# Kernel tuning notes

Hardware: AMD Instinct MI355X
Metric: run time of the kernel (lower is better)

## Reference

```python
import jax, jax.numpy as jnp
import numpy as np

N_NODES = 100000
N_EDGES = 3200000
D_IN = 256
D_HID = 97


def setup_inputs() -> dict:
    key = jax.random.key(0)
    k1, k2, k3, k4, k5, k6 = jax.random.split(key, 6)
    x = jax.random.normal(k1, (N_NODES, D_IN), dtype=jnp.float32)
    edge_index = jax.random.randint(k2, (2, N_EDGES), 0, N_NODES, dtype=jnp.int64)
    # GCNConv weights (stored as [in, out]) and biases
    W1 = jax.random.normal(k3, (D_IN, D_HID), dtype=jnp.float32) / np.sqrt(D_IN)
    b1 = jnp.zeros((D_HID,), dtype=jnp.float32)
    W2 = jax.random.normal(k4, (D_HID, D_HID), dtype=jnp.float32) / np.sqrt(D_HID)
    b2 = jnp.zeros((D_HID,), dtype=jnp.float32)
    return {"x": x, "edge_index": edge_index, "W1": W1, "b1": b1, "W2": W2, "b2": b2}


def reference(x, edge_index, W1, b1, W2, b2):
    # PyG GCNConv: add self-loops, symmetric degree normalization,
    # out[i] = sum_j norm_ij * (x[j] @ W) + b
    N = x.shape[0]
    self_idx = jnp.arange(N, dtype=edge_index.dtype)
    src = jnp.concatenate([edge_index[0], self_idx])  # source j
    dst = jnp.concatenate([edge_index[1], self_idx])  # target i
    deg = jax.ops.segment_sum(jnp.ones_like(dst, dtype=x.dtype), dst, num_segments=N)
    dinv = jnp.where(deg > 0, 1.0 / jnp.sqrt(deg), 0.0)
    norm = dinv[src] * dinv[dst]  # [E+N]

    def gcn(h, W, b):
        h = h @ W  # dense linear transform first (out_dim small)
        msg = h[src] * norm[:, None]  # gather + scale
        agg = jax.ops.segment_sum(msg, dst, num_segments=N)  # scatter-add
        return agg + b

    h = jax.nn.relu(gcn(x, W1, b1))
    out = gcn(h, W2, b2)
    return out
```

## Files before the change

### kernel.cpp

```cpp
#include <hip/hip_runtime.h>
#include <hip/hip_fp16.h>
#include <stdint.h>

#define D_IN 256
#define D_H  97
#define RST  96
#define NPB  512
#define NBMAX 256
#define CHUNK 4096
#define KP1  264
#define KP2  136

typedef _Float16 f16;
typedef f16   f16x8 __attribute__((ext_vector_type(8)));
typedef float f32x4 __attribute__((ext_vector_type(4)));

__device__ __forceinline__ int load_idx(const void* p, int is64, long long pos) {
  if (is64) return (int)(((const long long*)p)[pos]);
  return ((const int*)p)[pos];
}

__global__ void detect_kernel(const void* ei, long long E, int* flag) {
  const int* p32 = (const int*)ei;
  long long stride = E / 1024; if (stride < 1) stride = 1;
  int tid = threadIdx.x;
  int bad = 0;
  for (int s = 0; s < 4; ++s) {
    long long k = ((long long)tid * 4 + s) * stride;
    if (k < E) {
      if (p32[2 * k + 1] != 0) bad = 1;
    }
  }
  __shared__ int sh_bad;
  if (tid == 0) sh_bad = 0;
  __syncthreads();
  if (bad) atomicOr(&sh_bad, 1);
  __syncthreads();
  if (tid == 0) *flag = sh_bad ? 0 : 1;
}

__global__ __launch_bounds__(256) void bucket_scatter_direct(
    const void* ei, const int* __restrict__ flag, int* __restrict__ bcur,
    unsigned int* __restrict__ bsd, long long E, int nbuck, int cap) {
  __shared__ unsigned int packs[CHUNK];
  __shared__ unsigned char bkts[CHUNK];
  __shared__ int hist[NBMAX];
  __shared__ int gpos[NBMAX];
  __shared__ int cur[NBMAX];
  int tid = threadIdx.x;
  if (tid < NBMAX) { hist[tid] = 0; cur[tid] = 0; }
  __syncthreads();
  int f = *flag;
  long long base = (long long)blockIdx.x * CHUNK;
  int cnt = (int)((E - base < CHUNK) ? (E - base) : CHUNK);
  #pragma unroll 4
  for (int i = tid; i < cnt; i += 256) {
    long long e = base + i;
    int s = load_idx(ei, f, e);
    int d = load_idx(ei, f, E + e);
    int b = d >> 9;
    packs[i] = ((unsigned int)(d & (NPB - 1)) << 17) | (unsigned int)s;
    bkts[i] = (unsigned char)b;
    atomicAdd(&hist[b], 1);
  }
  __syncthreads();
  if (tid < nbuck) { int h = hist[tid]; if (h) gpos[tid] = atomicAdd(&bcur[tid], h); }
  __syncthreads();
  #pragma unroll 4
  for (int i = tid; i < cnt; i += 256) {
    int b = bkts[i];
    int r = atomicAdd(&cur[b], 1);
    int idx = gpos[b] + r;
    if (idx < cap) bsd[(size_t)b * cap + idx] = packs[i];
  }
}

__global__ void bucket_scan2(const int* __restrict__ bcur, int* __restrict__ bstart,
                             int* __restrict__ row_start, int N, int nbuck, int cap) {
  __shared__ int sh[256];
  int tid = threadIdx.x;
  int v = (tid < nbuck) ? min(bcur[tid], cap) : 0;
  sh[tid] = v;
  __syncthreads();
  for (int off = 1; off < 256; off <<= 1) {
    int a = (tid >= off) ? sh[tid - off] : 0;
    __syncthreads();
    sh[tid] += a;
    __syncthreads();
  }
  if (tid < nbuck) bstart[tid] = sh[tid] - v;
  if (tid == 255) { bstart[nbuck] = sh[255]; row_start[N] = sh[255]; }
}

__global__ __launch_bounds__(256) void bucket_finalize(
    const unsigned int* __restrict__ bsd, const int* __restrict__ bcur,
    const int* __restrict__ bstart,
    int* __restrict__ row_start, float* __restrict__ dinv,
    int* __restrict__ csr_src, int N, int cap) {
  __shared__ int h[NPB];
  __shared__ int rs[NPB];
  __shared__ int cur[NPB];
  __shared__ int wsum[4];
  int b = blockIdx.x, tid = threadIdx.x;
  int lane = tid & 63, wid = tid >> 6;
  h[2 * tid] = 0; h[2 * tid + 1] = 0;
  cur[2 * tid] = 0; cur[2 * tid + 1] = 0;
  __syncthreads();
  int d0 = b * cap;
  int cnt = min(bcur[b], cap);
  for (int i = tid; i < cnt; i += 256) atomicAdd(&h[bsd[d0 + i] >> 17], 1);
  __syncthreads();
  int a0 = h[2 * tid], a1 = h[2 * tid + 1];
  int tsum = a0 + a1;
  int incl = tsum;
  #pragma unroll
  for (int off = 1; off < 64; off <<= 1) {
    int n = __shfl_up(incl, off, 64);
    if (lane >= off) incl += n;
  }
  if (lane == 63) wsum[wid] = incl;
  __syncthreads();
  int woff = 0;
  for (int k = 0; k < wid; ++k) woff += wsum[k];
  int excl = woff + incl - tsum + bstart[b];
  rs[2 * tid] = excl;
  rs[2 * tid + 1] = excl + a0;
  int node0 = b * NPB;
  int n0 = node0 + 2 * tid, n1 = node0 + 2 * tid + 1;
  if (n0 < N) { row_start[n0] = excl;      dinv[n0] = rsqrtf((float)(a0 + 1)); }
  if (n1 < N) { row_start[n1] = excl + a0; dinv[n1] = rsqrtf((float)(a1 + 1)); }
  __syncthreads();
  for (int i = tid; i < cnt; i += 256) {
    unsigned int p = bsd[d0 + i];
    int r = p >> 17;
    int s = (int)(p & 0x1FFFFu);
    int rel = atomicAdd(&cur[r], 1);
    csr_src[rs[r] + rel] = s;
  }
}

__global__ void prep_kernel(const float* __restrict__ W1, const float* __restrict__ b1,
                            const float* __restrict__ W2, const float* __restrict__ b2,
                            f16* __restrict__ W1t, f16* __restrict__ W2t,
                            float* __restrict__ b1p, float* __restrict__ b2p) {
  int idx = blockIdx.x * blockDim.x + threadIdx.x;
  const int n1 = 112 * KP1, n2 = 112 * KP2;
  if (idx < n1) {
    int c = idx / KP1, k = idx % KP1;
    W1t[idx] = (f16)((c < D_H && k < 256) ? W1[k * D_H + c] : 0.f);
  } else if (idx < n1 + n2) {
    int j = idx - n1; int c = j / KP2, k = j % KP2;
    W2t[j] = (f16)((c < D_H && k < D_H) ? W2[k * D_H + c] : 0.f);
  } else if (idx < n1 + n2 + 128) {
    int c = idx - (n1 + n2);
    b1p[c] = (c < D_H) ? b1[c] : 0.0f;
  } else if (idx < n1 + n2 + 256) {
    int c = idx - (n1 + n2 + 128);
    b2p[c] = (c < D_H) ? b2[c] : 0.0f;
  }
}

template<int KI, int KP, bool IN_HALF>
__global__ __launch_bounds__(256) void mfma_gemm(
    const void* __restrict__ Av, const __half2* __restrict__ sideA,
    const f16* __restrict__ Wt, const float* __restrict__ dinv,
    __half* __restrict__ C, __half2* __restrict__ sideC, int N) {
  __shared__ f16 Bs[112 * KP];
  __shared__ f16 As[128 * 40];
  int tid = threadIdx.x;
  int wave = tid >> 6, lane = tid & 63;
  int row0 = blockIdx.x * 128;

  for (int i = tid * 8; i < 112 * KP; i += 2048)
    *(f16x8*)&Bs[i] = *(const f16x8*)&Wt[i];

  f32x4 acc[2][7];
  #pragma unroll
  for (int mg = 0; mg < 2; ++mg)
    #pragma unroll
    for (int cg = 0; cg < 7; ++cg)
      #pragma unroll
      for (int j = 0; j < 4; ++j) acc[mg][cg][j] = 0.f;

  for (int kb = 0; kb < KI; ++kb) {
    if (kb) __syncthreads();
    int k0 = kb * 32;
    if constexpr (!IN_HALF) {
      #pragma unroll
      for (int ii = 0; ii < 4; ++ii) {
        int i = tid + ii * 256;
        int row = i >> 3, col = (i & 7) * 4;
        int gr = row0 + row;
        float4 v = make_float4(0.f, 0.f, 0.f, 0.f);
        if (gr < N) v = *(const float4*)&((const float*)Av)[(size_t)gr * 256 + k0 + col];
        __half2* dst = (__half2*)&As[row * 40 + col];
        dst[0] = __floats2half2_rn(v.x, v.y);
        dst[1] = __floats2half2_rn(v.z, v.w);
      }
    } else {
      if (kb < KI - 1) {
        #pragma unroll
        for (int ii = 0; ii < 2; ++ii) {
          int i = tid + ii * 256;
          int row = i >> 2, col = (i & 3) * 8;
          int gr = row0 + row;
          f16x8 v;
          #pragma unroll
          for (int q = 0; q < 8; ++q) v[q] = (f16)0.f;
          if (gr < N) v = *(const f16x8*)&((const f16*)Av)[(size_t)gr * RST + k0 + col];
          *(f16x8*)&As[row * 40 + col] = v;
        }
      } else {
        if (tid < 128) {
          int gr = row0 + tid;
          f16 sv = (f16)0.f;
          if (gr < N) sv = ((const f16*)sideA)[2 * gr];
          f16* dst = &As[tid * 40];
          #pragma unroll
          for (int q = 0; q < 32; ++q) dst[q] = (f16)0.f;
          dst[0] = sv;
        }
      }
    }
    __syncthreads();
    int rbase = wave * 32 + (lane & 15);
    int kf = (lane >> 4) * 8;
    f16x8 a0 = *(const f16x8*)&As[rbase * 40 + kf];
    f16x8 a1 = *(const f16x8*)&As[(rbase + 16) * 40 + kf];
    #pragma unroll
    for (int cg = 0; cg < 7; ++cg) {
      f16x8 b = *(const f16x8*)&Bs[(cg * 16 + (lane & 15)) * KP + k0 + kf];
      acc[0][cg] = __builtin_amdgcn_mfma_f32_16x16x32_f16(a0, b, acc[0][cg], 0, 0, 0);
      acc[1][cg] = __builtin_amdgcn_mfma_f32_16x16x32_f16(a1, b, acc[1][cg], 0, 0, 0);
    }
  }
  int colb = lane & 15, rq = (lane >> 4) * 4;
  #pragma unroll
  for (int mg = 0; mg < 2; ++mg) {
    #pragma unroll
    for (int j = 0; j < 4; ++j) {
      int r = row0 + wave * 32 + mg * 16 + rq + j;
      if (r >= N) continue;
      float dv = dinv[r];
      #pragma unroll
      for (int cg = 0; cg < 7; ++cg) {
        int c = cg * 16 + colb;
        float val = acc[mg][cg][j] * dv;
        if (c < 96)       C[(size_t)r * RST + c] = __float2half(val);
        else if (c == 96) sideC[r] = __floats2half2_rn(val, 0.f);
      }
    }
  }
}

template<bool OUT_HALF, bool DO_RELU>
__global__ __launch_bounds__(256) void agg_kernel(
    const __half* __restrict__ t, const __half2* __restrict__ side,
    const int* __restrict__ csr_src, const int* __restrict__ row_start,
    const float* __restrict__ dinv, const float* __restrict__ bias,
    void* __restrict__ outp, __half2* __restrict__ side_out, int N) {
  int lane = threadIdx.x & 63;
  int node = blockIdx.x * (blockDim.x >> 6) + (threadIdx.x >> 6);
  if (node >= N || lane >= 49) return;
  const char* gbase = (lane < 48) ? (const char*)t + lane * 4 : (const char*)side;
  unsigned gscale = (lane < 48) ? (unsigned)(RST * 2) : 4u;
  auto GATHER = [&](int j) -> float2 {
    return __half22float2(*(const __half2*)(gbase + (size_t)((unsigned)j * gscale)));
  };
  int s = row_start[node], epd = row_start[node + 1];
  float di = dinv[node];
  float2 v = GATHER(node);
  float ax = v.x, ay = v.y;
  int e = s;
  while ((e & 3) && e < epd) {
    float2 u = GATHER(csr_src[e]);
    ax += u.x; ay += u.y; ++e;
  }
  for (; e + 8 <= epd; e += 8) {
    int4 q0 = *(const int4*)(csr_src + e);
    int4 q1 = *(const int4*)(csr_src + e + 4);
    float2 u0 = GATHER(q0.x), u1 = GATHER(q0.y), u2 = GATHER(q0.z), u3 = GATHER(q0.w);
    float2 u4 = GATHER(q1.x), u5 = GATHER(q1.y), u6 = GATHER(q1.z), u7 = GATHER(q1.w);
    ax += ((u0.x + u1.x) + (u2.x + u3.x)) + ((u4.x + u5.x) + (u6.x + u7.x));
    ay += ((u0.y + u1.y) + (u2.y + u3.y)) + ((u4.y + u5.y) + (u6.y + u7.y));
  }
  if (e + 4 <= epd) {
    int4 q0 = *(const int4*)(csr_src + e);
    float2 u0 = GATHER(q0.x), u1 = GATHER(q0.y), u2 = GATHER(q0.z), u3 = GATHER(q0.w);
    ax += (u0.x + u1.x) + (u2.x + u3.x);
    ay += (u0.y + u1.y) + (u2.y + u3.y);
    e += 4;
  }
  for (; e < epd; ++e) {
    float2 u = GATHER(csr_src[e]);
    ax += u.x; ay += u.y;
  }
  int c0 = 2 * lane;
  ax = ax * di + bias[c0];
  ay = ay * di + bias[c0 + 1];
  if (DO_RELU) { ax = fmaxf(ax, 0.f); ay = fmaxf(ay, 0.f); }
  if (OUT_HALF) {
    if (lane < 48) ((__half2*)((__half*)outp + (size_t)node * RST))[lane] = __floats2half2_rn(ax, ay);
    else           side_out[node] = __floats2half2_rn(ax, 0.f);
  } else {
    float* o = (float*)outp + (size_t)node * D_H;
    if (lane < 48) { o[c0] = ax; o[c0 + 1] = ay; }
    else           o[96] = ax;
  }
}

extern "C" void kernel_launch(void* const* d_in, const int* in_sizes, int n_in,
                              void* d_out, int out_size, void* d_ws, size_t ws_size,
                              hipStream_t stream) {
  const float* x  = (const float*)d_in[0];
  const void*  ei = d_in[1];
  const float* W1 = (const float*)d_in[2];
  const float* b1 = (const float*)d_in[3];
  const float* W2 = (const float*)d_in[4];
  const float* b2 = (const float*)d_in[5];
  int N = in_sizes[0] / D_IN;
  long long E = (long long)in_sizes[1] / 2;
  int nbuck = (N + NPB - 1) / NPB;
  int cap = (int)(E / nbuck) + 8192;

  char* base = (char*)d_ws;
  size_t off = 0;
  auto alloc = [&](size_t bytes) -> void* {
    void* p = base + off;
    off = (off + bytes + 255) & ~(size_t)255;
    return p;
  };
  int*    flag      = (int*)alloc(4);
  float*  dinv      = (float*)alloc((size_t)N * 4);
  int*    row_start = (int*)alloc((size_t)(N + 1) * 4);
  int*    bcur      = (int*)alloc((size_t)(nbuck + 1) * 4);
  int*    bstart    = (int*)alloc((size_t)(nbuck + 1) * 4);
  int*    csr_src   = (int*)alloc((size_t)E * 4);
  unsigned int* bsd = (unsigned int*)alloc((size_t)nbuck * cap * 4);
  f16*    W1t       = (f16*)alloc((size_t)112 * KP1 * 2);
  f16*    W2t       = (f16*)alloc((size_t)112 * KP2 * 2);
  float*  b1p       = (float*)alloc(128 * 4);
  float*  b2p       = (float*)alloc(128 * 4);
  __half* t1        = (__half*)alloc((size_t)N * RST * 2 + 256);
  __half2* sideT    = (__half2*)alloc((size_t)N * 4 + 256);
  __half* h1        = (__half*)alloc((size_t)N * RST * 2 + 256);
  __half2* sideH    = (__half2*)alloc((size_t)N * 4 + 256);

  hipMemsetAsync(bcur, 0, (size_t)(nbuck + 1) * 4, stream);
  detect_kernel<<<1, 256, 0, stream>>>(ei, E, flag);
  bucket_scatter_direct<<<(int)((E + CHUNK - 1) / CHUNK), 256, 0, stream>>>(
      ei, flag, bcur, bsd, E, nbuck, cap);
  bucket_scan2<<<1, 256, 0, stream>>>(bcur, bstart, row_start, N, nbuck, cap);
  bucket_finalize<<<nbuck, 256, 0, stream>>>(bsd, bcur, bstart, row_start, dinv, csr_src, N, cap);
  prep_kernel<<<(112 * KP1 + 112 * KP2 + 256 + 255) / 256, 256, 0, stream>>>(
      W1, b1, W2, b2, W1t, W2t, b1p, b2p);
  mfma_gemm<8, KP1, false><<<(N + 127) / 128, 256, 0, stream>>>(
      x, nullptr, W1t, dinv, t1, sideT, N);
  agg_kernel<true, true><<<(N + 3) / 4, 256, 0, stream>>>(t1, sideT, csr_src, row_start,
                                                          dinv, b1p, h1, sideH, N);
  mfma_gemm<4, KP2, true><<<(N + 127) / 128, 256, 0, stream>>>(
      h1, sideH, W2t, dinv, t1, sideT, N);
  agg_kernel<false, false><<<(N + 3) / 4, 256, 0, stream>>>(t1, sideT, csr_src, row_start,
                                                            dinv, b2p, d_out, nullptr, N);
}
```

Baseline: 374.9 us.

## Split hidden features into column slabs and aggregate each slab separately

The GEMMs now write the 97-wide hidden matrices as three 32-column fp16 slabs plus a separate scalar column. Aggregation runs one pass per slab, with 16 lanes per node, plus a thread-per-node pass for the extra column. The aim is to shrink each pass's gather working set so it fits better in cache. The cost is re-reading the CSR indices and row offsets four times per layer and launching more kernels.

Result: slower. 461.2 us (+23.0%).

```diff
diff --git a/kernel.cpp b/kernel.cpp
--- a/kernel.cpp
+++ b/kernel.cpp
@@ -4,7 +4,6 @@
 
 #define D_IN 256
 #define D_H  97
-#define RST  96
 #define NPB  512
 #define NBMAX 256
 #define CHUNK 4096
@@ -162,9 +161,12 @@
 
 template<int KI, int KP, bool IN_HALF>
 __global__ __launch_bounds__(256) void mfma_gemm(
-    const void* __restrict__ Av, const __half2* __restrict__ sideA,
+    const float* __restrict__ Af,
+    const f16* __restrict__ A0, const f16* __restrict__ A1,
+    const f16* __restrict__ A2, const f16* __restrict__ Aside,
     const f16* __restrict__ Wt, const float* __restrict__ dinv,
-    __half* __restrict__ C, __half2* __restrict__ sideC, int N) {
+    f16* __restrict__ C0, f16* __restrict__ C1, f16* __restrict__ C2,
+    f16* __restrict__ Cside, int N) {
   __shared__ f16 Bs[112 * KP];
   __shared__ f16 As[128 * 40];
   int tid = threadIdx.x;
@@ -192,13 +194,14 @@
         int row = i >> 3, col = (i & 7) * 4;
         int gr = row0 + row;
         float4 v = make_float4(0.f, 0.f, 0.f, 0.f);
-        if (gr < N) v = *(const float4*)&((const float*)Av)[(size_t)gr * 256 + k0 + col];
+        if (gr < N) v = *(const float4*)&Af[(size_t)gr * 256 + k0 + col];
         __half2* dst = (__half2*)&As[row * 40 + col];
         dst[0] = __floats2half2_rn(v.x, v.y);
         dst[1] = __floats2half2_rn(v.z, v.w);
       }
     } else {
-      if (kb < KI - 1) {
+      if (kb < 3) {
+        const f16* Ak = (kb == 0) ? A0 : (kb == 1) ? A1 : A2;
         #pragma unroll
         for (int ii = 0; ii < 2; ++ii) {
           int i = tid + ii * 256;
@@ -207,14 +210,14 @@
           f16x8 v;
           #pragma unroll
           for (int q = 0; q < 8; ++q) v[q] = (f16)0.f;
-          if (gr < N) v = *(const f16x8*)&((const f16*)Av)[(size_t)gr * RST + k0 + col];
+          if (gr < N) v = *(const f16x8*)&Ak[(size_t)gr * 32 + col];
           *(f16x8*)&As[row * 40 + col] = v;
         }
       } else {
         if (tid < 128) {
           int gr = row0 + tid;
           f16 sv = (f16)0.f;
-          if (gr < N) sv = ((const f16*)sideA)[2 * gr];
+          if (gr < N) sv = Aside[gr];
           f16* dst = &As[tid * 40];
           #pragma unroll
           for (int q = 0; q < 32; ++q) dst[q] = (f16)0.f;
@@ -245,68 +248,78 @@
       #pragma unroll
       for (int cg = 0; cg < 7; ++cg) {
         int c = cg * 16 + colb;
-        float val = acc[mg][cg][j] * dv;
-        if (c < 96)       C[(size_t)r * RST + c] = __float2half(val);
-        else if (c == 96) sideC[r] = __floats2half2_rn(val, 0.f);
+        f16 val = (f16)(acc[mg][cg][j] * dv);
+        if (cg < 2)       C0[(size_t)r * 32 + c]      = val;
+        else if (cg < 4)  C1[(size_t)r * 32 + c - 32] = val;
+        else if (cg < 6)  C2[(size_t)r * 32 + c - 64] = val;
+        else if (colb == 0) Cside[r] = val;
       }
     }
   }
 }
 
 template<bool OUT_HALF, bool DO_RELU>
-__global__ __launch_bounds__(256) void agg_kernel(
-    const __half* __restrict__ t, const __half2* __restrict__ side,
-    const int* __restrict__ csr_src, const int* __restrict__ row_start,
-    const float* __restrict__ dinv, const float* __restrict__ bias,
-    void* __restrict__ outp, __half2* __restrict__ side_out, int N) {
-  int lane = threadIdx.x & 63;
-  int node = blockIdx.x * (blockDim.x >> 6) + (threadIdx.x >> 6);
-  if (node >= N || lane >= 49) return;
-  const char* gbase = (lane < 48) ? (const char*)t + lane * 4 : (const char*)side;
-  unsigned gscale = (lane < 48) ? (unsigned)(RST * 2) : 4u;
-  auto GATHER = [&](int j) -> float2 {
-    return __half22float2(*(const __half2*)(gbase + (size_t)((unsigned)j * gscale)));
+__global__ __launch_bounds__(256) void agg_phase(
+    const __half* __restrict__ Tp, const int* __restrict__ csr_src,
+    const int* __restrict__ row_start, const float* __restrict__ dinv,
+    const float* __restrict__ bias, int p,
+    void* __restrict__ outp, int N) {
+  int tid = threadIdx.x;
+  int wave = tid >> 6, lane = tid & 63;
+  int g = lane >> 4, gl = lane & 15;
+  int node = blockIdx.x * 16 + wave * 4 + g;
+  bool act = node < N;
+  int nn = act ? node : 0;
+  int e = act ? row_start[nn] : 0;
+  int epd = act ? row_start[nn + 1] : 0;
+  auto G = [&](int j) -> float2 {
+    return __half22float2(((const __half2*)(Tp + (size_t)j * 32))[gl]);
   };
-  int s = row_start[node], epd = row_start[node + 1];
-  float di = dinv[node];
-  float2 v = GATHER(node);
-  float ax = v.x, ay = v.y;
-  int e = s;
-  while ((e & 3) && e < epd) {
-    float2 u = GATHER(csr_src[e]);
-    ax += u.x; ay += u.y; ++e;
-  }
-  for (; e + 8 <= epd; e += 8) {
-    int4 q0 = *(const int4*)(csr_src + e);
-    int4 q1 = *(const int4*)(csr_src + e + 4);
-    float2 u0 = GATHER(q0.x), u1 = GATHER(q0.y), u2 = GATHER(q0.z), u3 = GATHER(q0.w);
-    float2 u4 = GATHER(q1.x), u5 = GATHER(q1.y), u6 = GATHER(q1.z), u7 = GATHER(q1.w);
-    ax += ((u0.x + u1.x) + (u2.x + u3.x)) + ((u4.x + u5.x) + (u6.x + u7.x));
-    ay += ((u0.y + u1.y) + (u2.y + u3.y)) + ((u4.y + u5.y) + (u6.y + u7.y));
-  }
-  if (e + 4 <= epd) {
-    int4 q0 = *(const int4*)(csr_src + e);
-    float2 u0 = GATHER(q0.x), u1 = GATHER(q0.y), u2 = GATHER(q0.z), u3 = GATHER(q0.w);
-    ax += (u0.x + u1.x) + (u2.x + u3.x);
-    ay += (u0.y + u1.y) + (u2.y + u3.y);
-    e += 4;
+  float2 acc = make_float2(0.f, 0.f);
+  if (act) acc = G(nn);
+  for (; e + 4 <= epd; e += 4) {
+    int j0 = csr_src[e], j1 = csr_src[e + 1], j2 = csr_src[e + 2], j3 = csr_src[e + 3];
+    float2 u0 = G(j0), u1 = G(j1), u2 = G(j2), u3 = G(j3);
+    acc.x += (u0.x + u1.x) + (u2.x + u3.x);
+    acc.y += (u0.y + u1.y) + (u2.y + u3.y);
   }
   for (; e < epd; ++e) {
-    float2 u = GATHER(csr_src[e]);
-    ax += u.x; ay += u.y;
-  }
-  int c0 = 2 * lane;
-  ax = ax * di + bias[c0];
-  ay = ay * di + bias[c0 + 1];
+    float2 u = G(csr_src[e]);
+    acc.x += u.x; acc.y += u.y;
+  }
+  if (!act) return;
+  float di = dinv[nn];
+  int c0 = p * 32 + 2 * gl;
+  float ax = acc.x * di + bias[c0];
+  float ay = acc.y * di + bias[c0 + 1];
   if (DO_RELU) { ax = fmaxf(ax, 0.f); ay = fmaxf(ay, 0.f); }
   if (OUT_HALF) {
-    if (lane < 48) ((__half2*)((__half*)outp + (size_t)node * RST))[lane] = __floats2half2_rn(ax, ay);
-    else           side_out[node] = __floats2half2_rn(ax, 0.f);
+    ((__half2*)((__half*)outp + (size_t)nn * 32))[gl] = __floats2half2_rn(ax, ay);
   } else {
-    float* o = (float*)outp + (size_t)node * D_H;
-    if (lane < 48) { o[c0] = ax; o[c0 + 1] = ay; }
-    else           o[96] = ax;
-  }
+    float* o = (float*)outp + (size_t)nn * D_H + c0;
+    o[0] = ax; o[1] = ay;
+  }
+}
+
+template<bool OUT_HALF, bool DO_RELU>
+__global__ __launch_bounds__(256) void agg_side(
+    const f16* __restrict__ side, const int* __restrict__ csr_src,
+    const int* __restrict__ row_start, const float* __restrict__ dinv,
+    const float* __restrict__ bias, void* __restrict__ outp,
+    f16* __restrict__ side_out, int N) {
+  int n = blockIdx.x * 256 + threadIdx.x;
+  if (n >= N) return;
+  int e = row_start[n], epd = row_start[n + 1];
+  float a = (float)side[n];
+  for (; e + 4 <= epd; e += 4) {
+    int j0 = csr_src[e], j1 = csr_src[e + 1], j2 = csr_src[e + 2], j3 = csr_src[e + 3];
+    a += ((float)side[j0] + (float)side[j1]) + ((float)side[j2] + (float)side[j3]);
+  }
+  for (; e < epd; ++e) a += (float)side[csr_src[e]];
+  float v = a * dinv[n] + bias[96];
+  if (DO_RELU) v = fmaxf(v, 0.f);
+  if (OUT_HALF) side_out[n] = (f16)v;
+  else          ((float*)outp)[(size_t)n * D_H + 96] = v;
 }
 
 extern "C" void kernel_launch(void* const* d_in, const int* in_sizes, int n_in,
@@ -341,10 +354,14 @@
   f16*    W2t       = (f16*)alloc((size_t)112 * KP2 * 2);
   float*  b1p       = (float*)alloc(128 * 4);
   float*  b2p       = (float*)alloc(128 * 4);
-  __half* t1        = (__half*)alloc((size_t)N * RST * 2 + 256);
-  __half2* sideT    = (__half2*)alloc((size_t)N * 4 + 256);
-  __half* h1        = (__half*)alloc((size_t)N * RST * 2 + 256);
-  __half2* sideH    = (__half2*)alloc((size_t)N * 4 + 256);
+  f16*    T0        = (f16*)alloc((size_t)N * 32 * 2);
+  f16*    T1        = (f16*)alloc((size_t)N * 32 * 2);
+  f16*    T2        = (f16*)alloc((size_t)N * 32 * 2);
+  f16*    sT        = (f16*)alloc((size_t)N * 2);
+  f16*    H0        = (f16*)alloc((size_t)N * 32 * 2);
+  f16*    H1        = (f16*)alloc((size_t)N * 32 * 2);
+  f16*    H2        = (f16*)alloc((size_t)N * 32 * 2);
+  f16*    sH        = (f16*)alloc((size_t)N * 2);
 
   hipMemsetAsync(bcur, 0, (size_t)(nbuck + 1) * 4, stream);
   detect_kernel<<<1, 256, 0, stream>>>(ei, E, flag);
@@ -354,12 +371,22 @@
   bucket_finalize<<<nbuck, 256, 0, stream>>>(bsd, bcur, bstart, row_start, dinv, csr_src, N, cap);
   prep_kernel<<<(112 * KP1 + 112 * KP2 + 256 + 255) / 256, 256, 0, stream>>>(
       W1, b1, W2, b2, W1t, W2t, b1p, b2p);
-  mfma_gemm<8, KP1, false><<<(N + 127) / 128, 256, 0, stream>>>(
-      x, nullptr, W1t, dinv, t1, sideT, N);
-  agg_kernel<true, true><<<(N + 3) / 4, 256, 0, stream>>>(t1, sideT, csr_src, row_start,
-                                                          dinv, b1p, h1, sideH, N);
-  mfma_gemm<4, KP2, true><<<(N + 127) / 128, 256, 0, stream>>>(
-      h1, sideH, W2t, dinv, t1, sideT, N);
-  agg_kernel<false, false><<<(N + 3) / 4, 256, 0, stream>>>(t1, sideT, csr_src, row_start,
-                                                            dinv, b2p, d_out, nullptr, N);
-}
+
+  int gGemm = (N + 127) / 128;
+  int gPh   = (N + 15) / 16;
+  int gSd   = (N + 255) / 256;
+
+  mfma_gemm<8, KP1, false><<<gGemm, 256, 0, stream>>>(
+      x, nullptr, nullptr, nullptr, nullptr, W1t, dinv, T0, T1, T2, sT, N);
+  agg_phase<true, true><<<gPh, 256, 0, stream>>>((const __half*)T0, csr_src, row_start, dinv, b1p, 0, H0, N);
+  agg_phase<true, true><<<gPh, 256, 0, stream>>>((const __half*)T1, csr_src, row_start, dinv, b1p, 1, H1, N);
+  agg_phase<true, true><<<gPh, 256, 0, stream>>>((const __half*)T2, csr_src, row_start, dinv, b1p, 2, H2, N);
+  agg_side<true, true><<<gSd, 256, 0, stream>>>(sT, csr_src, row_start, dinv, b1p, nullptr, sH, N);
+
+  mfma_gemm<4, KP2, true><<<gGemm, 256, 0, stream>>>(
+      nullptr, H0, H1, H2, sH, W2t, dinv, T0, T1, T2, sT, N);
+  agg_phase<false, false><<<gPh, 256, 0, stream>>>((const __half*)T0, csr_src, row_start, dinv, b2p, 0, d_out, N);
+  agg_phase<false, false><<<gPh, 256, 0, stream>>>((const __half*)T1, csr_src, row_start, dinv, b2p, 1, d_out, N);
+  agg_phase<false, false><<<gPh, 256, 0, stream>>>((const __half*)T2, csr_src, row_start, dinv, b2p, 2, d_out, N);
+  agg_side<false, false><<<gSd, 256, 0, stream>>>(sT, csr_src, row_start, dinv, b2p, d_out, nullptr, N);
+}
```
